# Kernel optimization log

Measured on AMD Instinct MI355X. Metric: run time of the kernel, lower is better.

## Reference

```python
import jax, jax.numpy as jnp
import numpy as np

N = 50000       # nodes
E = 800000      # edges
D_IN, D_H, D_OUT = 64, 64, 32


def _glorot(key, fan_in, fan_out):
    lim = np.sqrt(6.0 / (fan_in + fan_out)).astype(np.float32)
    return jax.random.uniform(key, (fan_in, fan_out), jnp.float32, -lim, lim)


def setup_inputs() -> dict:
    key = jax.random.key(0)
    k = jax.random.split(key, 4)
    x = jax.random.normal(k[0], (N, D_IN), jnp.float32)
    edge_index = jax.random.randint(k[1], (2, E), 0, N, dtype=jnp.int64)
    W1 = _glorot(k[2], D_IN, D_H)
    b1 = jnp.zeros((D_H,), jnp.float32)
    W2 = _glorot(k[3], D_H, D_OUT)
    b2 = jnp.zeros((D_OUT,), jnp.float32)
    return {"x": x, "edge_index": edge_index, "W1": W1, "b1": b1, "W2": W2, "b2": b2}


def gcn_layer(x, W, b, src, dst, n):
    # PyG GCNConv: h = XW; add self-loops (weight 1); symmetric normalization
    # out[j] = sum_{i->j} h[i] / sqrt(deg(i) deg(j)) + h[j]/deg(j) + b
    h = x @ W                                           # [n, d_out]
    deg = jax.ops.segment_sum(jnp.ones((src.shape[0],), h.dtype), dst,
                              num_segments=n) + 1.0     # in-degree + self-loop
    dinv = jax.lax.rsqrt(deg)                           # deg >= 1
    norm = (dinv[src] * dinv[dst])[:, None]             # [E, 1]
    agg = jax.ops.segment_sum(h[src] * norm, dst, num_segments=n)
    # self-loop contribution: dinv[i]*dinv[i]*h[i]
    return agg + h * (dinv * dinv)[:, None] + b


def reference(x, edge_index, W1, b1, W2, b2):
    src, dst = edge_index[0], edge_index[1]
    h = gcn_layer(x, W1, b1, src, dst, N)
    h = jax.nn.relu(h)                                  # dropout is identity in eval mode
    return gcn_layer(h, W2, b2, src, dst, N)
```

## Files before the change

kernel.cpp:

```cpp
#include <hip/hip_runtime.h>
#include <hip/hip_fp16.h>
#include <cstddef>
#include <cstdint>

namespace {

constexpr int N  = 50000;
constexpr int E  = 800000;
constexpr int DH = 64;
constexpr int DO = 32;
constexpr int NB = (N + 255) / 256;
static_assert(N < 65536, "src packed as u16");
static_assert(NB <= 256, "phase-B single tile");

__device__ inline uint16_t f2bf(float f) {
    union { float f; uint32_t u; } c; c.f = f;
    uint32_t r = c.u + 0x7FFFu + ((c.u >> 16) & 1u);
    return (uint16_t)(r >> 16);
}
__device__ inline void bf2x(uint32_t p, float& a, float& b) {
    union { uint32_t u; float f; } c0, c1;
    c0.u = p << 16; c1.u = p & 0xFFFF0000u;
    a = c0.f; b = c1.f;
}

__global__ void k_zero(int* __restrict__ cnt) {
    int i = blockIdx.x * blockDim.x + threadIdx.x;
    if (i < N) cnt[i] = 0;
}

__global__ void k_count(const int* __restrict__ dst, int* __restrict__ cnt,
                        int* __restrict__ rank) {
    int e = blockIdx.x * blockDim.x + threadIdx.x;
    if (e < E) rank[e] = atomicAdd(&cnt[dst[e]], 1);
}

__launch_bounds__(256)
__global__ void k_gemm1(const float* __restrict__ X, const float* __restrict__ W1,
                        uint16_t* __restrict__ h1) {
    __shared__ float Ws[64 * DH];
    __shared__ float Xs[64 * 68];

    const int tid = threadIdx.x;
    const int rowBase = blockIdx.x * 64;

#pragma unroll
    for (int i = 0; i < 4; ++i) {
        const int q = tid + i * 256;
        reinterpret_cast<float4*>(Ws)[q] = reinterpret_cast<const float4*>(W1)[q];
    }
#pragma unroll
    for (int i = 0; i < 4; ++i) {
        const int q   = tid + i * 256;
        const int row = q >> 4;
        const int kq  = q & 15;
        const int gr  = min(rowBase + row, N - 1);
        const float4 v = *reinterpret_cast<const float4*>(X + (size_t)gr * 64 + kq * 4);
        *reinterpret_cast<float4*>(&Xs[row * 68 + kq * 4]) = v;
    }
    __syncthreads();

    const int rg = tid >> 4;
    const int cg = tid & 15;
    float acc[4][4];
#pragma unroll
    for (int r = 0; r < 4; ++r)
#pragma unroll
        for (int c = 0; c < 4; ++c) acc[r][c] = 0.0f;

#pragma unroll
    for (int k4 = 0; k4 < 16; ++k4) {
        const int k = k4 * 4;
        float xr[4][4];
#pragma unroll
        for (int r = 0; r < 4; ++r) {
            const float4 v = *reinterpret_cast<const float4*>(&Xs[(rg * 4 + r) * 68 + k]);
            xr[r][0] = v.x; xr[r][1] = v.y; xr[r][2] = v.z; xr[r][3] = v.w;
        }
#pragma unroll
        for (int i = 0; i < 4; ++i) {
            const float4 v = *reinterpret_cast<const float4*>(&Ws[(k + i) * DH + cg * 4]);
            const float wv[4] = {v.x, v.y, v.z, v.w};
#pragma unroll
            for (int r = 0; r < 4; ++r)
#pragma unroll
                for (int c = 0; c < 4; ++c) acc[r][c] += xr[r][i] * wv[c];
        }
    }

#pragma unroll
    for (int r = 0; r < 4; ++r) {
        const int row = rowBase + rg * 4 + r;
        if (row < N) {
            uint2 o;
            o.x = (uint32_t)f2bf(acc[r][0]) | ((uint32_t)f2bf(acc[r][1]) << 16);
            o.y = (uint32_t)f2bf(acc[r][2]) | ((uint32_t)f2bf(acc[r][3]) << 16);
            *reinterpret_cast<uint2*>(&h1[(size_t)row * DH + cg * 4]) = o;
        }
    }
}

__launch_bounds__(256)
__global__ void k_gemm2(const float* __restrict__ Y, const float* __restrict__ W2,
                        uint16_t* __restrict__ h2) {
    __shared__ float Ws[64 * DO];
    __shared__ float Xs[64 * 68];

    const int tid = threadIdx.x;
    const int rowBase = blockIdx.x * 64;

#pragma unroll
    for (int i = 0; i < 2; ++i) {
        const int q = tid + i * 256;
        reinterpret_cast<float4*>(Ws)[q] = reinterpret_cast<const float4*>(W2)[q];
    }
#pragma unroll
    for (int i = 0; i < 4; ++i) {
        const int q   = tid + i * 256;
        const int row = q >> 4;
        const int kq  = q & 15;
        const int gr  = min(rowBase + row, N - 1);
        const float4 v = *reinterpret_cast<const float4*>(Y + (size_t)gr * 64 + kq * 4);
        *reinterpret_cast<float4*>(&Xs[row * 68 + kq * 4]) = v;
    }
    __syncthreads();

    const int rg = tid >> 4;
    const int cg = tid & 15;
    float acc[4][2];
#pragma unroll
    for (int r = 0; r < 4; ++r) { acc[r][0] = 0.0f; acc[r][1] = 0.0f; }

#pragma unroll
    for (int k4 = 0; k4 < 16; ++k4) {
        const int k = k4 * 4;
        float xr[4][4];
#pragma unroll
        for (int r = 0; r < 4; ++r) {
            const float4 v = *reinterpret_cast<const float4*>(&Xs[(rg * 4 + r) * 68 + k]);
            xr[r][0] = v.x; xr[r][1] = v.y; xr[r][2] = v.z; xr[r][3] = v.w;
        }
#pragma unroll
        for (int i = 0; i < 4; ++i) {
            const float2 v = *reinterpret_cast<const float2*>(&Ws[(k + i) * DO + cg * 2]);
#pragma unroll
            for (int r = 0; r < 4; ++r) {
                acc[r][0] += xr[r][i] * v.x;
                acc[r][1] += xr[r][i] * v.y;
            }
        }
    }

#pragma unroll
    for (int r = 0; r < 4; ++r) {
        const int row = rowBase + rg * 4 + r;
        if (row < N) {
            const uint32_t o = (uint32_t)f2bf(acc[r][0]) | ((uint32_t)f2bf(acc[r][1]) << 16);
            *reinterpret_cast<uint32_t*>(&h2[(size_t)row * DO + cg * 2]) = o;
        }
    }
}

__global__ void k_scanA(const int* __restrict__ cnt, int* __restrict__ incl,
                        int* __restrict__ bsum) {
    __shared__ int ts[256];
    const int t = threadIdx.x;
    const int i = blockIdx.x * 256 + t;
    const int v = (i < N) ? cnt[i] : 0;
    ts[t] = v;
    __syncthreads();
#pragma unroll
    for (int off = 1; off < 256; off <<= 1) {
        const int u = (t >= off) ? ts[t - off] : 0;
        __syncthreads();
        ts[t] += u;
        __syncthreads();
    }
    if (i < N) incl[i] = ts[t];
    if (t == 255) bsum[blockIdx.x] = ts[255];
}

__global__ void k_scanB(int* __restrict__ bsum) {
    __shared__ int ts[256];
    const int t = threadIdx.x;
    const int v = (t < NB) ? bsum[t] : 0;
    ts[t] = v;
    __syncthreads();
#pragma unroll
    for (int off = 1; off < 256; off <<= 1) {
        const int u = (t >= off) ? ts[t - off] : 0;
        __syncthreads();
        ts[t] += u;
        __syncthreads();
    }
    if (t < NB) bsum[t] = ts[t] - v;
}

__global__ void k_scanC(const int* __restrict__ cnt, const int* __restrict__ incl,
                        const int* __restrict__ bbase, int* __restrict__ rowptr,
                        float* __restrict__ dinv) {
    const int i = blockIdx.x * 256 + threadIdx.x;
    if (i >= N) return;
    const int c    = cnt[i];
    const int excl = bbase[blockIdx.x] + incl[i] - c;
    rowptr[i] = excl;
    dinv[i]   = rsqrtf((float)(c + 1));
    if (i == N - 1) rowptr[N] = excl + c;
}

__global__ void k_fill(const int* __restrict__ src, const int* __restrict__ dst,
                       const int* __restrict__ rank, const int* __restrict__ rowptr,
                       const float* __restrict__ dinv, uint32_t* __restrict__ epack) {
    int e = blockIdx.x * blockDim.x + threadIdx.x;
    if (e >= E) return;
    const int s = src[e], d = dst[e];
    const int pos = rowptr[d] + rank[e];
    const float wn = dinv[s] * dinv[d];
    const uint16_t hb = __half_as_ushort(__float2half(wn));
    epack[pos] = (uint32_t)s | ((uint32_t)hb << 16);
}

__launch_bounds__(256)
__global__ void k_agg1(const int* __restrict__ rowptr, const uint32_t* __restrict__ epack,
                       const uint16_t* __restrict__ h1, const float* __restrict__ dinv,
                       const float* __restrict__ b1, float* __restrict__ y1) {
    const int gtid = blockIdx.x * 256 + threadIdx.x;
    const int n    = gtid >> 6;
    const int lane = threadIdx.x & 63;
    if (n >= N) return;
    const int g  = lane >> 3;
    const int sl = lane & 7;
    const int beg = rowptr[n], end = rowptr[n + 1];

    float acc[8] = {0.f, 0.f, 0.f, 0.f, 0.f, 0.f, 0.f, 0.f};
    for (int j = beg; j < end; j += 8) {
        const int jj = j + g;
        int s = 0; float wn = 0.0f;
        if (jj < end) {
            const uint32_t w = epack[jj];
            s  = (int)(w & 0xFFFFu);
            wn = __half2float(__ushort_as_half((uint16_t)(w >> 16)));
        }
        const uint4 v = *reinterpret_cast<const uint4*>(h1 + (size_t)s * DH + sl * 8);
        float f0, f1;
        bf2x(v.x, f0, f1); acc[0] += wn * f0; acc[1] += wn * f1;
        bf2x(v.y, f0, f1); acc[2] += wn * f0; acc[3] += wn * f1;
        bf2x(v.z, f0, f1); acc[4] += wn * f0; acc[5] += wn * f1;
        bf2x(v.w, f0, f1); acc[6] += wn * f0; acc[7] += wn * f1;
    }
#pragma unroll
    for (int m = 8; m < 64; m <<= 1)
#pragma unroll
        for (int k = 0; k < 8; ++k) acc[k] += __shfl_xor(acc[k], m);

    if (g < 2) {
        const float di = dinv[n], d2 = di * di;
        const int fb = sl * 8 + g * 4;
        const uint2 sv = *reinterpret_cast<const uint2*>(h1 + (size_t)n * DH + fb);
        float s0, s1, s2, s3;
        bf2x(sv.x, s0, s1); bf2x(sv.y, s2, s3);
        const float4 bv = *reinterpret_cast<const float4*>(b1 + fb);
        float4 o;
        o.x = fmaxf(acc[g * 4 + 0] + s0 * d2 + bv.x, 0.f);
        o.y = fmaxf(acc[g * 4 + 1] + s1 * d2 + bv.y, 0.f);
        o.z = fmaxf(acc[g * 4 + 2] + s2 * d2 + bv.z, 0.f);
        o.w = fmaxf(acc[g * 4 + 3] + s3 * d2 + bv.w, 0.f);
        *reinterpret_cast<float4*>(y1 + (size_t)n * DH + fb) = o;
    }
}

__global__ void k_agg2(const int* __restrict__ rowptr, const uint32_t* __restrict__ epack,
                       const uint16_t* __restrict__ h2, const float* __restrict__ dinv,
                       const float* __restrict__ b2, float* __restrict__ out) {
    const int gtid = blockIdx.x * blockDim.x + threadIdx.x;
    const int n    = gtid >> 6;
    const int lane = gtid & 63;
    if (n >= N) return;
    const int g  = lane >> 2;
    const int sl = lane & 3;
    const int beg = rowptr[n], end = rowptr[n + 1];

    float acc[8] = {0.f, 0.f, 0.f, 0.f, 0.f, 0.f, 0.f, 0.f};
    for (int j = beg; j < end; j += 16) {
        const int jj = j + g;
        int s = 0; float wn = 0.0f;
        if (jj < end) {
            const uint32_t w = epack[jj];
            s  = (int)(w & 0xFFFFu);
            wn = __half2float(__ushort_as_half((uint16_t)(w >> 16)));
        }
        const uint4 v = *reinterpret_cast<const uint4*>(h2 + (size_t)s * DO + sl * 8);
        float f0, f1;
        bf2x(v.x, f0, f1); acc[0] += wn * f0; acc[1] += wn * f1;
        bf2x(v.y, f0, f1); acc[2] += wn * f0; acc[3] += wn * f1;
        bf2x(v.z, f0, f1); acc[4] += wn * f0; acc[5] += wn * f1;
        bf2x(v.w, f0, f1); acc[6] += wn * f0; acc[7] += wn * f1;
    }
#pragma unroll
    for (int m = 4; m < 64; m <<= 1)
#pragma unroll
        for (int k = 0; k < 8; ++k) acc[k] += __shfl_xor(acc[k], m);

    if (g < 2) {
        const float di = dinv[n], d2 = di * di;
        const int fb = sl * 8 + g * 4;
        const uint2 sv = *reinterpret_cast<const uint2*>(h2 + (size_t)n * DO + fb);
        float s0, s1, s2, s3;
        bf2x(sv.x, s0, s1); bf2x(sv.y, s2, s3);
        const float4 bv = *reinterpret_cast<const float4*>(b2 + fb);
        float4 o;
        o.x = acc[g * 4 + 0] + s0 * d2 + bv.x;
        o.y = acc[g * 4 + 1] + s1 * d2 + bv.y;
        o.z = acc[g * 4 + 2] + s2 * d2 + bv.z;
        o.w = acc[g * 4 + 3] + s3 * d2 + bv.w;
        *reinterpret_cast<float4*>(out + (size_t)n * DO + fb) = o;
    }
}

template <typename T>
T* alignp(char*& p, size_t count) {
    uintptr_t u = ((uintptr_t)p + 63) & ~(uintptr_t)63;
    p = (char*)(u + count * sizeof(T));
    return (T*)u;
}

}

extern "C" void kernel_launch(void* const* d_in, const int* in_sizes, int n_in,
                              void* d_out, int out_size, void* d_ws, size_t ws_size,
                              hipStream_t stream) {
    const float* x   = (const float*)d_in[0];
    const int*   ei  = (const int*)d_in[1];
    const float* W1  = (const float*)d_in[2];
    const float* b1  = (const float*)d_in[3];
    const float* W2  = (const float*)d_in[4];
    const float* b2  = (const float*)d_in[5];
    float* out = (float*)d_out;

    const int* src = ei;
    const int* dst = ei + E;

    char* p = (char*)d_ws;
    int*      cnt    = alignp<int>(p, N);
    int*      rowptr = alignp<int>(p, N + 1);
    int*      rank   = alignp<int>(p, E);
    float*    dinv   = alignp<float>(p, N);
    int*      incl   = alignp<int>(p, N);
    int*      bsum   = alignp<int>(p, NB);
    uint32_t* epack  = alignp<uint32_t>(p, E);
    uint16_t* h1     = alignp<uint16_t>(p, (size_t)N * DH);
    float*    y1     = alignp<float>(p, (size_t)N * DH);
    uint16_t* h2     = alignp<uint16_t>(p, (size_t)N * DO);

    hipLaunchKernelGGL(k_zero, dim3((N + 255) / 256), dim3(256), 0, stream, cnt);
    hipLaunchKernelGGL(k_count, dim3((E + 255) / 256), dim3(256), 0, stream,
                       dst, cnt, rank);
    hipLaunchKernelGGL(k_gemm1, dim3((N + 63) / 64), dim3(256), 0, stream, x, W1, h1);
    hipLaunchKernelGGL(k_scanA, dim3(NB), dim3(256), 0, stream, cnt, incl, bsum);
    hipLaunchKernelGGL(k_scanB, dim3(1), dim3(256), 0, stream, bsum);
    hipLaunchKernelGGL(k_scanC, dim3(NB), dim3(256), 0, stream, cnt, incl, bsum,
                       rowptr, dinv);
    hipLaunchKernelGGL(k_fill, dim3((E + 255) / 256), dim3(256), 0, stream,
                       src, dst, rank, rowptr, dinv, epack);
    hipLaunchKernelGGL(k_agg1, dim3((N * 64 + 255) / 256), dim3(256), 0, stream,
                       rowptr, epack, h1, dinv, b1, y1);
    hipLaunchKernelGGL(k_gemm2, dim3((N + 63) / 64), dim3(256), 0, stream, y1, W2, h2);
    hipLaunchKernelGGL(k_agg2, dim3((N * 64 + 255) / 256), dim3(256), 0, stream,
                       rowptr, epack, h2, dinv, b2, out);
}
```

Measured before the change: 152.1 us.

## Merge scan phases B/C and fuse edge fill with first GEMM

Folds the single-block scan of block sums into the per-node finalize kernel, so every block redundantly rescans the block-sum array instead of running a separate launch. Also merges the CSR fill kernel and the first feature GEMM into one launch whose leading blocks do edge scatter and trailing blocks do the GEMM tiles. This cuts the launch count from ten to eight and lets the independent GEMM overlap with the scatter. In exchange the fill blocks now reserve the GEMM's shared memory, which can lower occupancy for that part, and each scan block repeats a small scan.

```diff
diff --git a/kernel.cpp b/kernel.cpp
--- a/kernel.cpp
+++ b/kernel.cpp
@@ -10,8 +10,10 @@
 constexpr int DH = 64;
 constexpr int DO = 32;
 constexpr int NB = (N + 255) / 256;
+constexpr int FB = (E + 255) / 256;
+constexpr int GB = (N + 63) / 64;
 static_assert(N < 65536, "src packed as u16");
-static_assert(NB <= 256, "phase-B single tile");
+static_assert(NB <= 256, "single-tile block scan");
 
 __device__ inline uint16_t f2bf(float f) {
     union { float f; uint32_t u; } c; c.f = f;
@@ -33,132 +35,6 @@
                         int* __restrict__ rank) {
     int e = blockIdx.x * blockDim.x + threadIdx.x;
     if (e < E) rank[e] = atomicAdd(&cnt[dst[e]], 1);
-}
-
-__launch_bounds__(256)
-__global__ void k_gemm1(const float* __restrict__ X, const float* __restrict__ W1,
-                        uint16_t* __restrict__ h1) {
-    __shared__ float Ws[64 * DH];
-    __shared__ float Xs[64 * 68];
-
-    const int tid = threadIdx.x;
-    const int rowBase = blockIdx.x * 64;
-
-#pragma unroll
-    for (int i = 0; i < 4; ++i) {
-        const int q = tid + i * 256;
-        reinterpret_cast<float4*>(Ws)[q] = reinterpret_cast<const float4*>(W1)[q];
-    }
-#pragma unroll
-    for (int i = 0; i < 4; ++i) {
-        const int q   = tid + i * 256;
-        const int row = q >> 4;
-        const int kq  = q & 15;
-        const int gr  = min(rowBase + row, N - 1);
-        const float4 v = *reinterpret_cast<const float4*>(X + (size_t)gr * 64 + kq * 4);
-        *reinterpret_cast<float4*>(&Xs[row * 68 + kq * 4]) = v;
-    }
-    __syncthreads();
-
-    const int rg = tid >> 4;
-    const int cg = tid & 15;
-    float acc[4][4];
-#pragma unroll
-    for (int r = 0; r < 4; ++r)
-#pragma unroll
-        for (int c = 0; c < 4; ++c) acc[r][c] = 0.0f;
-
-#pragma unroll
-    for (int k4 = 0; k4 < 16; ++k4) {
-        const int k = k4 * 4;
-        float xr[4][4];
-#pragma unroll
-        for (int r = 0; r < 4; ++r) {
-            const float4 v = *reinterpret_cast<const float4*>(&Xs[(rg * 4 + r) * 68 + k]);
-            xr[r][0] = v.x; xr[r][1] = v.y; xr[r][2] = v.z; xr[r][3] = v.w;
-        }
-#pragma unroll
-        for (int i = 0; i < 4; ++i) {
-            const float4 v = *reinterpret_cast<const float4*>(&Ws[(k + i) * DH + cg * 4]);
-            const float wv[4] = {v.x, v.y, v.z, v.w};
-#pragma unroll
-            for (int r = 0; r < 4; ++r)
-#pragma unroll
-                for (int c = 0; c < 4; ++c) acc[r][c] += xr[r][i] * wv[c];
-        }
-    }
-
-#pragma unroll
-    for (int r = 0; r < 4; ++r) {
-        const int row = rowBase + rg * 4 + r;
-        if (row < N) {
-            uint2 o;
-            o.x = (uint32_t)f2bf(acc[r][0]) | ((uint32_t)f2bf(acc[r][1]) << 16);
-            o.y = (uint32_t)f2bf(acc[r][2]) | ((uint32_t)f2bf(acc[r][3]) << 16);
-            *reinterpret_cast<uint2*>(&h1[(size_t)row * DH + cg * 4]) = o;
-        }
-    }
-}
-
-__launch_bounds__(256)
-__global__ void k_gemm2(const float* __restrict__ Y, const float* __restrict__ W2,
-                        uint16_t* __restrict__ h2) {
-    __shared__ float Ws[64 * DO];
-    __shared__ float Xs[64 * 68];
-
-    const int tid = threadIdx.x;
-    const int rowBase = blockIdx.x * 64;
-
-#pragma unroll
-    for (int i = 0; i < 2; ++i) {
-        const int q = tid + i * 256;
-        reinterpret_cast<float4*>(Ws)[q] = reinterpret_cast<const float4*>(W2)[q];
-    }
-#pragma unroll
-    for (int i = 0; i < 4; ++i) {
-        const int q   = tid + i * 256;
-        const int row = q >> 4;
-        const int kq  = q & 15;
-        const int gr  = min(rowBase + row, N - 1);
-        const float4 v = *reinterpret_cast<const float4*>(Y + (size_t)gr * 64 + kq * 4);
-        *reinterpret_cast<float4*>(&Xs[row * 68 + kq * 4]) = v;
-    }
-    __syncthreads();
-
-    const int rg = tid >> 4;
-    const int cg = tid & 15;
-    float acc[4][2];
-#pragma unroll
-    for (int r = 0; r < 4; ++r) { acc[r][0] = 0.0f; acc[r][1] = 0.0f; }
-
-#pragma unroll
-    for (int k4 = 0; k4 < 16; ++k4) {
-        const int k = k4 * 4;
-        float xr[4][4];
-#pragma unroll
-        for (int r = 0; r < 4; ++r) {
-            const float4 v = *reinterpret_cast<const float4*>(&Xs[(rg * 4 + r) * 68 + k]);
-            xr[r][0] = v.x; xr[r][1] = v.y; xr[r][2] = v.z; xr[r][3] = v.w;
-        }
-#pragma unroll
-        for (int i = 0; i < 4; ++i) {
-            const float2 v = *reinterpret_cast<const float2*>(&Ws[(k + i) * DO + cg * 2]);
-#pragma unroll
-            for (int r = 0; r < 4; ++r) {
-                acc[r][0] += xr[r][i] * v.x;
-                acc[r][1] += xr[r][i] * v.y;
-            }
-        }
-    }
-
-#pragma unroll
-    for (int r = 0; r < 4; ++r) {
-        const int row = rowBase + rg * 4 + r;
-        if (row < N) {
-            const uint32_t o = (uint32_t)f2bf(acc[r][0]) | ((uint32_t)f2bf(acc[r][1]) << 16);
-            *reinterpret_cast<uint32_t*>(&h2[(size_t)row * DO + cg * 2]) = o;
-        }
-    }
 }
 
 __global__ void k_scanA(const int* __restrict__ cnt, int* __restrict__ incl,
@@ -180,11 +56,12 @@
     if (t == 255) bsum[blockIdx.x] = ts[255];
 }
 
-__global__ void k_scanB(int* __restrict__ bsum) {
+__global__ void k_scanBC(const int* __restrict__ cnt, const int* __restrict__ incl,
+                         const int* __restrict__ bsum, int* __restrict__ rowptr,
+                         float* __restrict__ dinv) {
     __shared__ int ts[256];
     const int t = threadIdx.x;
-    const int v = (t < NB) ? bsum[t] : 0;
-    ts[t] = v;
+    ts[t] = (t < NB) ? bsum[t] : 0;
     __syncthreads();
 #pragma unroll
     for (int off = 1; off < 256; off <<= 1) {
@@ -193,31 +70,155 @@
         ts[t] += u;
         __syncthreads();
     }
-    if (t < NB) bsum[t] = ts[t] - v;
-}
-
-__global__ void k_scanC(const int* __restrict__ cnt, const int* __restrict__ incl,
-                        const int* __restrict__ bbase, int* __restrict__ rowptr,
-                        float* __restrict__ dinv) {
-    const int i = blockIdx.x * 256 + threadIdx.x;
+    const int base = (blockIdx.x == 0) ? 0 : ts[blockIdx.x - 1];
+    const int i = blockIdx.x * 256 + t;
     if (i >= N) return;
     const int c    = cnt[i];
-    const int excl = bbase[blockIdx.x] + incl[i] - c;
+    const int excl = base + incl[i] - c;
     rowptr[i] = excl;
     dinv[i]   = rsqrtf((float)(c + 1));
     if (i == N - 1) rowptr[N] = excl + c;
 }
 
-__global__ void k_fill(const int* __restrict__ src, const int* __restrict__ dst,
-                       const int* __restrict__ rank, const int* __restrict__ rowptr,
-                       const float* __restrict__ dinv, uint32_t* __restrict__ epack) {
-    int e = blockIdx.x * blockDim.x + threadIdx.x;
-    if (e >= E) return;
-    const int s = src[e], d = dst[e];
-    const int pos = rowptr[d] + rank[e];
-    const float wn = dinv[s] * dinv[d];
-    const uint16_t hb = __half_as_ushort(__float2half(wn));
-    epack[pos] = (uint32_t)s | ((uint32_t)hb << 16);
+__launch_bounds__(256, 4)
+__global__ void k_fillg(const int* __restrict__ src, const int* __restrict__ dst,
+                        const int* __restrict__ rank, const int* __restrict__ rowptr,
+                        const float* __restrict__ dinv, uint32_t* __restrict__ epack,
+                        const float* __restrict__ X, const float* __restrict__ W1,
+                        uint16_t* __restrict__ h1) {
+    __shared__ float Ws[64 * DH];
+    __shared__ float Xs[64 * 68];
+
+    if (blockIdx.x < FB) {
+        const int e = blockIdx.x * 256 + threadIdx.x;
+        if (e < E) {
+            const int s = src[e], d = dst[e];
+            const int pos = rowptr[d] + rank[e];
+            const float wn = dinv[s] * dinv[d];
+            const uint16_t hb = __half_as_ushort(__float2half(wn));
+            epack[pos] = (uint32_t)s | ((uint32_t)hb << 16);
+        }
+        return;
+    }
+
+    const int tid = threadIdx.x;
+    const int rowBase = (blockIdx.x - FB) * 64;
+
+#pragma unroll
+    for (int i = 0; i < 4; ++i) {
+        const int q = tid + i * 256;
+        reinterpret_cast<float4*>(Ws)[q] = reinterpret_cast<const float4*>(W1)[q];
+    }
+#pragma unroll
+    for (int i = 0; i < 4; ++i) {
+        const int q   = tid + i * 256;
+        const int row = q >> 4;
+        const int kq  = q & 15;
+        const int gr  = min(rowBase + row, N - 1);
+        const float4 v = *reinterpret_cast<const float4*>(X + (size_t)gr * 64 + kq * 4);
+        *reinterpret_cast<float4*>(&Xs[row * 68 + kq * 4]) = v;
+    }
+    __syncthreads();
+
+    const int rg = tid >> 4;
+    const int cg = tid & 15;
+    float acc[4][4];
+#pragma unroll
+    for (int r = 0; r < 4; ++r)
+#pragma unroll
+        for (int c = 0; c < 4; ++c) acc[r][c] = 0.0f;
+
+#pragma unroll
+    for (int k4 = 0; k4 < 16; ++k4) {
+        const int k = k4 * 4;
+        float xr[4][4];
+#pragma unroll
+        for (int r = 0; r < 4; ++r) {
+            const float4 v = *reinterpret_cast<const float4*>(&Xs[(rg * 4 + r) * 68 + k]);
+            xr[r][0] = v.x; xr[r][1] = v.y; xr[r][2] = v.z; xr[r][3] = v.w;
+        }
+#pragma unroll
+        for (int i = 0; i < 4; ++i) {
+            const float4 v = *reinterpret_cast<const float4*>(&Ws[(k + i) * DH + cg * 4]);
+            const float wv[4] = {v.x, v.y, v.z, v.w};
+#pragma unroll
+            for (int r = 0; r < 4; ++r)
+#pragma unroll
+                for (int c = 0; c < 4; ++c) acc[r][c] += xr[r][i] * wv[c];
+        }
+    }
+
+#pragma unroll
+    for (int r = 0; r < 4; ++r) {
+        const int row = rowBase + rg * 4 + r;
+        if (row < N) {
+            uint2 o;
+            o.x = (uint32_t)f2bf(acc[r][0]) | ((uint32_t)f2bf(acc[r][1]) << 16);
+            o.y = (uint32_t)f2bf(acc[r][2]) | ((uint32_t)f2bf(acc[r][3]) << 16);
+            *reinterpret_cast<uint2*>(&h1[(size_t)row * DH + cg * 4]) = o;
+        }
+    }
+}
+
+__launch_bounds__(256)
+__global__ void k_gemm2(const float* __restrict__ Y, const float* __restrict__ W2,
+                        uint16_t* __restrict__ h2) {
+    __shared__ float Ws[64 * DO];
+    __shared__ float Xs[64 * 68];
+
+    const int tid = threadIdx.x;
+    const int rowBase = blockIdx.x * 64;
+
+#pragma unroll
+    for (int i = 0; i < 2; ++i) {
+        const int q = tid + i * 256;
+        reinterpret_cast<float4*>(Ws)[q] = reinterpret_cast<const float4*>(W2)[q];
+    }
+#pragma unroll
+    for (int i = 0; i < 4; ++i) {
+        const int q   = tid + i * 256;
+        const int row = q >> 4;
+        const int kq  = q & 15;
+        const int gr  = min(rowBase + row, N - 1);
+        const float4 v = *reinterpret_cast<const float4*>(Y + (size_t)gr * 64 + kq * 4);
+        *reinterpret_cast<float4*>(&Xs[row * 68 + kq * 4]) = v;
+    }
+    __syncthreads();
+
+    const int rg = tid >> 4;
+    const int cg = tid & 15;
+    float acc[4][2];
+#pragma unroll
+    for (int r = 0; r < 4; ++r) { acc[r][0] = 0.0f; acc[r][1] = 0.0f; }
+
+#pragma unroll
+    for (int k4 = 0; k4 < 16; ++k4) {
+        const int k = k4 * 4;
+        float xr[4][4];
+#pragma unroll
+        for (int r = 0; r < 4; ++r) {
+            const float4 v = *reinterpret_cast<const float4*>(&Xs[(rg * 4 + r) * 68 + k]);
+            xr[r][0] = v.x; xr[r][1] = v.y; xr[r][2] = v.z; xr[r][3] = v.w;
+        }
+#pragma unroll
+        for (int i = 0; i < 4; ++i) {
+            const float2 v = *reinterpret_cast<const float2*>(&Ws[(k + i) * DO + cg * 2]);
+#pragma unroll
+            for (int r = 0; r < 4; ++r) {
+                acc[r][0] += xr[r][i] * v.x;
+                acc[r][1] += xr[r][i] * v.y;
+            }
+        }
+    }
+
+#pragma unroll
+    for (int r = 0; r < 4; ++r) {
+        const int row = rowBase + rg * 4 + r;
+        if (row < N) {
+            const uint32_t o = (uint32_t)f2bf(acc[r][0]) | ((uint32_t)f2bf(acc[r][1]) << 16);
+            *reinterpret_cast<uint32_t*>(&h2[(size_t)row * DO + cg * 2]) = o;
+        }
+    }
 }
 
 __launch_bounds__(256)
@@ -355,13 +356,11 @@
     hipLaunchKernelGGL(k_zero, dim3((N + 255) / 256), dim3(256), 0, stream, cnt);
     hipLaunchKernelGGL(k_count, dim3((E + 255) / 256), dim3(256), 0, stream,
                        dst, cnt, rank);
-    hipLaunchKernelGGL(k_gemm1, dim3((N + 63) / 64), dim3(256), 0, stream, x, W1, h1);
     hipLaunchKernelGGL(k_scanA, dim3(NB), dim3(256), 0, stream, cnt, incl, bsum);
-    hipLaunchKernelGGL(k_scanB, dim3(1), dim3(256), 0, stream, bsum);
-    hipLaunchKernelGGL(k_scanC, dim3(NB), dim3(256), 0, stream, cnt, incl, bsum,
-                       rowptr, dinv);
-    hipLaunchKernelGGL(k_fill, dim3((E + 255) / 256), dim3(256), 0, stream,
-                       src, dst, rank, rowptr, dinv, epack);
+    hipLaunchKernelGGL(k_scanBC, dim3(NB), dim3(256), 0, stream,
+                       cnt, incl, bsum, rowptr, dinv);
+    hipLaunchKernelGGL(k_fillg, dim3(FB + GB), dim3(256), 0, stream,
+                       src, dst, rank, rowptr, dinv, epack, x, W1, h1);
     hipLaunchKernelGGL(k_agg1, dim3((N * 64 + 255) / 256), dim3(256), 0, stream,
                        rowptr, epack, h1, dinv, b1, y1);
     hipLaunchKernelGGL(k_gemm2, dim3((N + 63) / 64), dim3(256), 0, stream, y1, W2, h2);
```

After: 479.4 us. 215% more time.
